# Kernel tuning notes

Measured on AMD Instinct MI355X. Metric: run time of the kernel, lower is better.

## Reference

```python
import jax, jax.numpy as jnp
import numpy as np

# search space constants
NUM_INIT_NODES = 2
NUM_NODE_INPUTS = 2
NUM_STEPS = 4
NUM_NODES = NUM_INIT_NODES + NUM_STEPS  # 6
NUM_CELL_GROUPS = 2
NUM_PRIMITIVES = 8
OP_DIM = 48
OP_HID = 48
GCN_DIMS = [128, 128]
BATCH = 32768
N_EDGE = NUM_NODE_INPUTS * NUM_STEPS  # 8


def setup_inputs() -> dict:
    key = jax.random.key(0)
    ks = jax.random.split(key, 8)
    archs = jax.random.randint(ks[0], (BATCH, NUM_CELL_GROUPS, 2, N_EDGE), 0, 6, dtype=jnp.int64 if jax.config.jax_enable_x64 else jnp.int32)
    init_node_emb = jax.random.normal(ks[1], (NUM_INIT_NODES, NUM_NODE_INPUTS * OP_DIM), dtype=jnp.float32)
    op_emb = jax.random.normal(ks[2], (NUM_PRIMITIVES, OP_DIM), dtype=jnp.float32)
    x_hidden_w = jax.random.normal(ks[3], (NUM_NODE_INPUTS * OP_DIM, OP_HID), dtype=jnp.float32) * 0.1
    x_hidden_b = jax.random.normal(ks[4], (OP_HID,), dtype=jnp.float32) * 0.1
    gcn_w1 = jax.random.normal(ks[5], (OP_HID, GCN_DIMS[0]), dtype=jnp.float32) * 0.1
    gcn_w2 = jax.random.normal(ks[6], (GCN_DIMS[0], GCN_DIMS[1]), dtype=jnp.float32) * 0.1
    return {"archs": archs, "init_node_emb": init_node_emb, "op_emb": op_emb,
            "x_hidden_w": x_hidden_w, "x_hidden_b": x_hidden_b,
            "gcn_w1": gcn_w1, "gcn_w2": gcn_w2}


def _get_adj_dense(prev_nodes):
    # prev_nodes: [B2, n_edge] int; scatter-add counts into [B2, N, N]
    b2 = prev_nodes.shape[0]
    t_nodes = jnp.repeat(jnp.arange(NUM_INIT_NODES, NUM_NODES), NUM_NODE_INPUTS)  # [n_edge]
    bidx = jnp.arange(b2)[:, None]
    adj = jnp.zeros((b2, NUM_NODES, NUM_NODES), dtype=jnp.float32)
    adj = adj.at[bidx, t_nodes[None, :], prev_nodes].add(1.0)
    return adj


def reference(archs, init_node_emb, op_emb, x_hidden_w, x_hidden_b, gcn_w1, gcn_w2):
    b, n_cg, _, n_edge = archs.shape
    # dense adjacency per (batch, cell group)
    adjs = _get_adj_dense(archs[:, :, 0, :].reshape(-1, n_edge))
    adjs = adjs.reshape(b, n_cg, NUM_NODES, NUM_NODES)  # [b, g, N, N]
    # op embedding lookup -> intermediate node embeddings
    op_inds = archs[:, :, 1, :]                          # [b, g, n_edge]
    op_embs = op_emb[op_inds]                            # [b, g, n_edge, op_dim]
    inter = op_embs.reshape(b, n_cg, NUM_STEPS, NUM_NODE_INPUTS * OP_DIM)
    init = jnp.broadcast_to(init_node_emb[None, None], (b, n_cg, NUM_INIT_NODES, NUM_NODE_INPUTS * OP_DIM))
    node_embs = jnp.concatenate([init, inter], axis=2)   # [b, g, N, 2*op_dim]
    y = jnp.einsum('bgnd,df->bgnf', node_embs, x_hidden_w) + x_hidden_b  # [b,g,N,op_hid]
    # GCN layers: adj @ (y @ W); relu between layers (not after last); dropout=0 (eval)
    for i, w in enumerate([gcn_w1, gcn_w2]):
        y = jnp.einsum('bgnm,bgmf->bgnf', adjs, jnp.einsum('bgnd,df->bgnf', y, w))
        if i != 1:
            y = jax.nn.relu(y)
    y = jnp.mean(y[:, :, NUM_INIT_NODES:, :], axis=2)    # [b, g, out]
    return y.reshape(b, -1)                               # [b, g*out]
```

## Files before the change

kernel.cpp:

```cpp
#include <hip/hip_runtime.h>
#include <hip/hip_bf16.h>


typedef __attribute__((ext_vector_type(8))) short  bhalf8;
typedef __attribute__((ext_vector_type(4))) float  f32x4;

#define TAB_ROW 132

__device__ __forceinline__ unsigned int bf16rne(float x) {
  unsigned int u = __builtin_bit_cast(unsigned int, x);
  return (u + 0x7FFFu + ((u >> 16) & 1u)) >> 16;
}


__global__ __launch_bounds__(256) void prep_kernel(
    const float* __restrict__ init_emb,
    const float* __restrict__ op_emb,
    const float* __restrict__ wx,
    const float* __restrict__ xb,
    const float* __restrict__ w1,
    const float* __restrict__ w2,
    float* __restrict__ R,
    unsigned short* __restrict__ w2t)
{
  const int tid = threadIdx.x;
  const int b = blockIdx.x;

  if (b < 64) {
    int idx = b * 256 + tid;
    int f = idx >> 7, k = idx & 127;
    w2t[f * 128 + k] = (unsigned short)bf16rne(0.25f * w2[k * 128 + f]);
    return;
  }

  __shared__ float swx[96 * 48];
  __shared__ float sw1[48 * 128];
  __shared__ float smisc[6 * 48 + 2 * 96 + 48];
  __shared__ float sU[14][48];

  for (int i = tid; i < 96 * 48; i += 256) swx[i] = wx[i];
  for (int i = tid; i < 48 * 128; i += 256) sw1[i] = w1[i];
  for (int i = tid; i < 288; i += 256) smisc[i] = op_emb[i];
  if (tid < 192) smisc[288 + tid] = init_emb[tid];
  if (tid < 48)  smisc[480 + tid] = xb[tid];
  __syncthreads();

  const float* sob   = smisc;
  const float* sinit = smisc + 288;
  const float* sxb   = smisc + 480;

  for (int idx = tid; idx < 14 * 48; idx += 256) {
    int row = idx / 48, k = idx - row * 48;
    float s;
    if (row < 6) {
      s = sxb[k];
      for (int j = 0; j < 48; ++j) s += sob[row * 48 + j] * swx[j * 48 + k];
    } else if (row < 12) {
      s = 0.f;
      for (int j = 0; j < 48; ++j) s += sob[(row - 6) * 48 + j] * swx[(48 + j) * 48 + k];
    } else {
      s = sxb[k];
      for (int j = 0; j < 96; ++j) s += sinit[(row - 12) * 96 + j] * swx[j * 48 + k];
    }
    sU[row][k] = s;
  }
  __syncthreads();

  for (int idx = tid; idx < 14 * 128; idx += 256) {
    int row = idx >> 7, f = idx & 127;
    float s = 0.f;
    for (int k = 0; k < 48; ++k) s += sU[row][k] * sw1[k * 128 + f];
    R[idx] = s;
  }
}

__global__ __launch_bounds__(256, 4) void main_kernel(
    const int* __restrict__ archs,
    const float* __restrict__ R,
    const unsigned short* __restrict__ w2t,
    float* __restrict__ out)
{
  __shared__ float sT[38 * TAB_ROW];

  const int tid  = threadIdx.x;
  const int lane = tid & 63;
  const int wv   = tid >> 6;
  const int rbase = blockIdx.x * 64 + wv * 16;

  const int mrow = lane & 15;
  const int kq   = lane >> 4;
  const int r    = rbase + mrow;

  const int* ar = archs + r * 16;
  int4 pv0 = *(const int4*)(ar);
  int4 pv1 = *(const int4*)(ar + 4);
  int4 op0 = *(const int4*)(ar + 8);
  int4 op1 = *(const int4*)(ar + 12);

  for (int idx = tid; idx < 38 * 128; idx += 256) {
    int row = idx >> 7, f = idx & 127;
    float v;
    if (row < 36) {
      int o1 = row / 6, o2 = row - o1 * 6;
      v = R[o1 * 128 + f] + R[(6 + o2) * 128 + f];
    } else {
      v = R[(row - 24) * 128 + f];
    }
    sT[row * TAB_ROW + f] = v;
  }
  __syncthreads();

  int soff0 = (op0.x * 6 + op0.y) * TAB_ROW;
  int soff1 = (op0.z * 6 + op0.w) * TAB_ROW;
  int soff2 = (op1.x * 6 + op1.y) * TAB_ROW;
  int soff3 = (op1.z * 6 + op1.w) * TAB_ROW;
  const int s36 = 36 * TAB_ROW, s37 = 37 * TAB_ROW;

  int prev[8] = {pv0.x, pv0.y, pv0.z, pv0.w, pv1.x, pv1.y, pv1.z, pv1.w};
  int aoff[4], boff[4];
  float cf[4];
#pragma unroll
  for (int t = 0; t < 4; ++t) {
    int pa = prev[2 * t], pb = prev[2 * t + 1];
    aoff[t] = (pa == 0) ? s36 : (pa == 1) ? s37 : (pa == 2) ? soff0
            : (pa == 3) ? soff1 : (pa == 4) ? soff2 : soff3;
    boff[t] = (pb == 0) ? s36 : (pb == 1) ? s37 : (pb == 2) ? soff0
            : (pb == 3) ? soff1 : (pb == 4) ? soff2 : soff3;
    int c = 0;
#pragma unroll
    for (int e = 0; e < 8; ++e) c += (prev[e] == t + 2) ? 1 : 0;
    cf[t] = (float)c;
  }

  bhalf8 Af[4];
#pragma unroll
  for (int kc = 0; kc < 4; ++kc) {
    const int d = kq * 8 + kc * 32;
    unsigned int pk[4];
#pragma unroll
    for (int half = 0; half < 2; ++half) {
      f32x4 v = {0.f, 0.f, 0.f, 0.f};
      const int dd = d + half * 4;
#pragma unroll
      for (int t = 0; t < 4; ++t) {
        f32x4 a = *(const f32x4*)&sT[aoff[t] + dd];
        f32x4 b = *(const f32x4*)&sT[boff[t] + dd];
        f32x4 y = a + b;
        y[0] = fmaxf(y[0], 0.f); y[1] = fmaxf(y[1], 0.f);
        y[2] = fmaxf(y[2], 0.f); y[3] = fmaxf(y[3], 0.f);
        v += cf[t] * y;
      }
      pk[2 * half]     = bf16rne(v[0]) | (bf16rne(v[1]) << 16);
      pk[2 * half + 1] = bf16rne(v[2]) | (bf16rne(v[3]) << 16);
    }
    Af[kc] = __builtin_bit_cast(bhalf8, *(__attribute__((ext_vector_type(4))) unsigned int*)pk);
  }

#pragma unroll
  for (int nt = 0; nt < 8; ++nt) {
    f32x4 acc = {0.f, 0.f, 0.f, 0.f};
    const unsigned short* wb = w2t + (nt * 16 + mrow) * 128 + kq * 8;
#pragma unroll
    for (int kc = 0; kc < 4; ++kc) {
      bhalf8 Bf = *(const bhalf8*)(wb + kc * 32);
      acc = __builtin_amdgcn_mfma_f32_16x16x32_bf16(Af[kc], Bf, acc, 0, 0, 0);
    }
#pragma unroll
    for (int j = 0; j < 4; ++j)
      out[(rbase + kq * 4 + j) * 128 + nt * 16 + mrow] = acc[j];
  }
}

extern "C" void kernel_launch(void* const* d_in, const int* in_sizes, int n_in,
                              void* d_out, int out_size, void* d_ws, size_t ws_size,
                              hipStream_t stream) {
  const int*   archs  = (const int*)d_in[0];
  const float* init_e = (const float*)d_in[1];
  const float* op_e   = (const float*)d_in[2];
  const float* wx     = (const float*)d_in[3];
  const float* xb     = (const float*)d_in[4];
  const float* w1     = (const float*)d_in[5];
  const float* w2     = (const float*)d_in[6];

  float*          R   = (float*)d_ws;
  unsigned short* w2t = (unsigned short*)((char*)d_ws + 8192);

  prep_kernel<<<65, 256, 0, stream>>>(init_e, op_e, wx, xb, w1, w2, R, w2t);
  main_kernel<<<1024, 256, 0, stream>>>(archs, R, w2t, (float*)d_out);
}
```

Baseline: 109.4 us.

## Precompute full pair table through W2 so main kernel only gathers rows

Result: faster. 98.04 us (median of 2 runs) (-10.4%).

```diff
diff --git a/kernel.cpp b/kernel.cpp
--- a/kernel.cpp
+++ b/kernel.cpp
@@ -1,17 +1,12 @@
 #include <hip/hip_runtime.h>
-#include <hip/hip_bf16.h>
 
 
-typedef __attribute__((ext_vector_type(8))) short  bhalf8;
-typedef __attribute__((ext_vector_type(4))) float  f32x4;
+typedef __attribute__((ext_vector_type(4))) float f32x4;
 
-#define TAB_ROW 132
-
-__device__ __forceinline__ unsigned int bf16rne(float x) {
-  unsigned int u = __builtin_bit_cast(unsigned int, x);
-  return (u + 0x7FFFu + ((u >> 16) & 1u)) >> 16;
-}
-
+#define NSYM 38
+#define NPAIR (NSYM * NSYM)
+#define G_ROWS_PER_BLOCK 16
+#define PREP_BLOCKS ((NPAIR + G_ROWS_PER_BLOCK - 1) / G_ROWS_PER_BLOCK)
 
 __global__ __launch_bounds__(256) void prep_kernel(
     const float* __restrict__ init_emb,
@@ -20,23 +15,17 @@
     const float* __restrict__ xb,
     const float* __restrict__ w1,
     const float* __restrict__ w2,
-    float* __restrict__ R,
-    unsigned short* __restrict__ w2t)
+    float* __restrict__ G)
 {
-  const int tid = threadIdx.x;
-  const int b = blockIdx.x;
-
-  if (b < 64) {
-    int idx = b * 256 + tid;
-    int f = idx >> 7, k = idx & 127;
-    w2t[f * 128 + k] = (unsigned short)bf16rne(0.25f * w2[k * 128 + f]);
-    return;
-  }
-
   __shared__ float swx[96 * 48];
   __shared__ float sw1[48 * 128];
   __shared__ float smisc[6 * 48 + 2 * 96 + 48];
   __shared__ float sU[14][48];
+  __shared__ float sR[14 * 128];
+  __shared__ float sV[16][128];
+
+  const int tid = threadIdx.x;
+  const int qbase = blockIdx.x * G_ROWS_PER_BLOCK;
 
   for (int i = tid; i < 96 * 48; i += 256) swx[i] = wx[i];
   for (int i = tid; i < 48 * 128; i += 256) sw1[i] = w1[i];
@@ -70,104 +59,95 @@
     int row = idx >> 7, f = idx & 127;
     float s = 0.f;
     for (int k = 0; k < 48; ++k) s += sU[row][k] * sw1[k * 128 + f];
-    R[idx] = s;
+    sR[idx] = s;
+  }
+  __syncthreads();
+
+  for (int idx = tid; idx < 16 * 128; idx += 256) {
+    int i = idx >> 7, f = idx & 127;
+    int q = qbase + i; if (q > NPAIR - 1) q = NPAIR - 1;
+    int x = q / NSYM, y = q - x * NSYM;
+    float tx, ty;
+    if (x < 36) { int o1 = x / 6, o2 = x - o1 * 6; tx = sR[o1 * 128 + f] + sR[(6 + o2) * 128 + f]; }
+    else        { tx = sR[(x - 24) * 128 + f]; }
+    if (y < 36) { int o1 = y / 6, o2 = y - o1 * 6; ty = sR[o1 * 128 + f] + sR[(6 + o2) * 128 + f]; }
+    else        { ty = sR[(y - 24) * 128 + f]; }
+    sV[i][f] = 0.25f * fmaxf(tx + ty, 0.f);
+  }
+  __syncthreads();
+
+  const int fq = tid & 31;
+  const int slot0 = tid >> 5;
+#pragma unroll
+  for (int pass = 0; pass < 2; ++pass) {
+    const int slot = slot0 + pass * 8;
+    f32x4 acc = {0.f, 0.f, 0.f, 0.f};
+    const float* w2p = w2 + fq * 4;
+    for (int k = 0; k < 128; ++k) {
+      f32x4 w = *(const f32x4*)(w2p + k * 128);
+      acc += sV[slot][k] * w;
+    }
+    const int q = qbase + slot;
+    if (q < NPAIR) *(f32x4*)(G + q * 128 + fq * 4) = acc;
   }
 }
 
 __global__ __launch_bounds__(256, 4) void main_kernel(
     const int* __restrict__ archs,
-    const float* __restrict__ R,
-    const unsigned short* __restrict__ w2t,
+    const float* __restrict__ G,
     float* __restrict__ out)
 {
-  __shared__ float sT[38 * TAB_ROW];
+  __shared__ int   soff[64][4];
+  __shared__ float scf[64][4];
 
-  const int tid  = threadIdx.x;
-  const int lane = tid & 63;
-  const int wv   = tid >> 6;
-  const int rbase = blockIdx.x * 64 + wv * 16;
+  const int tid = threadIdx.x;
+  const int rbase = blockIdx.x * 64;
 
-  const int mrow = lane & 15;
-  const int kq   = lane >> 4;
-  const int r    = rbase + mrow;
+  if (tid < 64) {
+    const int* ar = archs + (rbase + tid) * 16;
+    int4 pv0 = *(const int4*)(ar);
+    int4 pv1 = *(const int4*)(ar + 4);
+    int4 op0 = *(const int4*)(ar + 8);
+    int4 op1 = *(const int4*)(ar + 12);
 
-  const int* ar = archs + r * 16;
-  int4 pv0 = *(const int4*)(ar);
-  int4 pv1 = *(const int4*)(ar + 4);
-  int4 op0 = *(const int4*)(ar + 8);
-  int4 op1 = *(const int4*)(ar + 12);
+    const int sp0 = op0.x * 6 + op0.y;
+    const int sp1 = op0.z * 6 + op0.w;
+    const int sp2 = op1.x * 6 + op1.y;
+    const int sp3 = op1.z * 6 + op1.w;
 
-  for (int idx = tid; idx < 38 * 128; idx += 256) {
-    int row = idx >> 7, f = idx & 127;
-    float v;
-    if (row < 36) {
-      int o1 = row / 6, o2 = row - o1 * 6;
-      v = R[o1 * 128 + f] + R[(6 + o2) * 128 + f];
-    } else {
-      v = R[(row - 24) * 128 + f];
+    int prev[8] = {pv0.x, pv0.y, pv0.z, pv0.w, pv1.x, pv1.y, pv1.z, pv1.w};
+#pragma unroll
+    for (int t = 0; t < 4; ++t) {
+      int pa = prev[2 * t], pb = prev[2 * t + 1];
+      int a = (pa == 0) ? 36 : (pa == 1) ? 37 : (pa == 2) ? sp0
+            : (pa == 3) ? sp1 : (pa == 4) ? sp2 : sp3;
+      int b = (pb == 0) ? 36 : (pb == 1) ? 37 : (pb == 2) ? sp0
+            : (pb == 3) ? sp1 : (pb == 4) ? sp2 : sp3;
+      int c = 0;
+#pragma unroll
+      for (int e = 0; e < 8; ++e) c += (prev[e] == t + 2) ? 1 : 0;
+      soff[tid][t] = (a * NSYM + b) * 128;
+      scf[tid][t]  = (float)c;
     }
-    sT[row * TAB_ROW + f] = v;
   }
   __syncthreads();
 
-  int soff0 = (op0.x * 6 + op0.y) * TAB_ROW;
-  int soff1 = (op0.z * 6 + op0.w) * TAB_ROW;
-  int soff2 = (op1.x * 6 + op1.y) * TAB_ROW;
-  int soff3 = (op1.z * 6 + op1.w) * TAB_ROW;
-  const int s36 = 36 * TAB_ROW, s37 = 37 * TAB_ROW;
-
-  int prev[8] = {pv0.x, pv0.y, pv0.z, pv0.w, pv1.x, pv1.y, pv1.z, pv1.w};
-  int aoff[4], boff[4];
-  float cf[4];
+  const int lane32 = tid & 31;
+  const int grp    = tid >> 5;
 #pragma unroll
-  for (int t = 0; t < 4; ++t) {
-    int pa = prev[2 * t], pb = prev[2 * t + 1];
-    aoff[t] = (pa == 0) ? s36 : (pa == 1) ? s37 : (pa == 2) ? soff0
-            : (pa == 3) ? soff1 : (pa == 4) ? soff2 : soff3;
-    boff[t] = (pb == 0) ? s36 : (pb == 1) ? s37 : (pb == 2) ? soff0
-            : (pb == 3) ? soff1 : (pb == 4) ? soff2 : soff3;
-    int c = 0;
-#pragma unroll
-    for (int e = 0; e < 8; ++e) c += (prev[e] == t + 2) ? 1 : 0;
-    cf[t] = (float)c;
-  }
-
-  bhalf8 Af[4];
-#pragma unroll
-  for (int kc = 0; kc < 4; ++kc) {
-    const int d = kq * 8 + kc * 32;
-    unsigned int pk[4];
-#pragma unroll
-    for (int half = 0; half < 2; ++half) {
-      f32x4 v = {0.f, 0.f, 0.f, 0.f};
-      const int dd = d + half * 4;
-#pragma unroll
-      for (int t = 0; t < 4; ++t) {
-        f32x4 a = *(const f32x4*)&sT[aoff[t] + dd];
-        f32x4 b = *(const f32x4*)&sT[boff[t] + dd];
-        f32x4 y = a + b;
-        y[0] = fmaxf(y[0], 0.f); y[1] = fmaxf(y[1], 0.f);
-        y[2] = fmaxf(y[2], 0.f); y[3] = fmaxf(y[3], 0.f);
-        v += cf[t] * y;
-      }
-      pk[2 * half]     = bf16rne(v[0]) | (bf16rne(v[1]) << 16);
-      pk[2 * half + 1] = bf16rne(v[2]) | (bf16rne(v[3]) << 16);
-    }
-    Af[kc] = __builtin_bit_cast(bhalf8, *(__attribute__((ext_vector_type(4))) unsigned int*)pk);
-  }
-
-#pragma unroll
-  for (int nt = 0; nt < 8; ++nt) {
-    f32x4 acc = {0.f, 0.f, 0.f, 0.f};
-    const unsigned short* wb = w2t + (nt * 16 + mrow) * 128 + kq * 8;
-#pragma unroll
-    for (int kc = 0; kc < 4; ++kc) {
-      bhalf8 Bf = *(const bhalf8*)(wb + kc * 32);
-      acc = __builtin_amdgcn_mfma_f32_16x16x32_bf16(Af[kc], Bf, acc, 0, 0, 0);
-    }
-#pragma unroll
-    for (int j = 0; j < 4; ++j)
-      out[(rbase + kq * 4 + j) * 128 + nt * 16 + mrow] = acc[j];
+  for (int rr = 0; rr < 8; ++rr) {
+    const int row = grp * 8 + rr;
+    int4  o4 = *(const int4*)&soff[row][0];
+    f32x4 c4 = *(const f32x4*)&scf[row][0];
+    f32x4 v0 = *(const f32x4*)(G + o4.x + lane32 * 4);
+    f32x4 v1 = *(const f32x4*)(G + o4.y + lane32 * 4);
+    f32x4 v2 = *(const f32x4*)(G + o4.z + lane32 * 4);
+    f32x4 v3 = *(const f32x4*)(G + o4.w + lane32 * 4);
+    f32x4 acc = c4.x * v0;
+    acc += c4.y * v1;
+    acc += c4.z * v2;
+    acc += c4.w * v3;
+    *(f32x4*)(out + (rbase + row) * 128 + lane32 * 4) = acc;
   }
 }
 
@@ -182,9 +162,8 @@
   const float* w1     = (const float*)d_in[5];
   const float* w2     = (const float*)d_in[6];
 
-  float*          R   = (float*)d_ws;
-  unsigned short* w2t = (unsigned short*)((char*)d_ws + 8192);
+  float* G = (float*)d_ws;
 
-  prep_kernel<<<65, 256, 0, stream>>>(init_e, op_e, wx, xb, w1, w2, R, w2t);
-  main_kernel<<<1024, 256, 0, stream>>>(archs, R, w2t, (float*)d_out);
+  prep_kernel<<<PREP_BLOCKS, 256, 0, stream>>>(init_e, op_e, wx, xb, w1, w2, G);
+  main_kernel<<<1024, 256, 0, stream>>>(archs, G, (float*)d_out);
 }
```
